# Kernel optimization log

Measured on AMD Instinct MI355X. Metric: run time of the kernel, lower is better.

## Reference

```python
import jax, jax.numpy as jnp
import numpy as np

B, S, D, H = 4, 2048, 1024, 16
DEPTH = D // H
NEG = -1e9


def setup_inputs() -> dict:
    key = jax.random.key(0)
    ks = jax.random.split(key, 9)
    scale = 1.0 / np.sqrt(D)
    x = jax.random.normal(ks[0], (B, S, D), dtype=jnp.float32)
    # causal additive mask: 1 where future positions (masked), 0 elsewhere
    mask = jnp.triu(jnp.ones((S, S), dtype=jnp.float32), k=1)[None, None, :, :]
    wq = jax.random.normal(ks[1], (D, D), dtype=jnp.float32) * scale
    bq = jnp.zeros((D,), dtype=jnp.float32)
    wk = jax.random.normal(ks[2], (D, D), dtype=jnp.float32) * scale
    bk = jnp.zeros((D,), dtype=jnp.float32)
    wv = jax.random.normal(ks[3], (D, D), dtype=jnp.float32) * scale
    bv = jnp.zeros((D,), dtype=jnp.float32)
    wo = jax.random.normal(ks[4], (D, D), dtype=jnp.float32) * scale
    bo = jnp.zeros((D,), dtype=jnp.float32)
    return {"x": x, "mask": mask, "wq": wq, "bq": bq, "wk": wk, "bk": bk,
            "wv": wv, "bv": bv, "wo": wo, "bo": bo}


def _split_heads(t):
    # [B, S, D] -> [B, H, S, depth]
    return t.reshape(B, S, H, DEPTH).transpose(0, 2, 1, 3)


def reference(x, mask, wq, bq, wk, bk, wv, bv, wo, bo):
    q = _split_heads(x @ wq.T + bq)
    k = _split_heads(x @ wk.T + bk)
    v = _split_heads(x @ wv.T + bv)
    scores = jnp.einsum('bhqd,bhkd->bhqk', q, k) / jnp.sqrt(jnp.float32(DEPTH))
    scores = scores + mask * NEG
    attn = jax.nn.softmax(scores, axis=-1)
    out = jnp.einsum('bhqk,bhkd->bhqd', attn, v)  # [B, H, S, depth]
    out = out.transpose(0, 2, 1, 3).reshape(B, S, D)
    return out @ wo.T + bo
```

## Files before the change

### kernel.cpp

```cpp
#include <hip/hip_runtime.h>
#include <hip/hip_bf16.h>
#include <stdint.h>

typedef __attribute__((ext_vector_type(8))) short short8;
typedef __attribute__((ext_vector_type(4))) float f32x4;
typedef __attribute__((ext_vector_type(16))) float f32x16;

#define AS1 __attribute__((address_space(1)))
#define AS3 __attribute__((address_space(3)))

constexpr int Bc = 4, Sc = 2048, Dc = 1024, Hc = 16;

__device__ __forceinline__ unsigned short f2b(float x) {
  __hip_bfloat16 h = __float2bfloat16(x);
  return *reinterpret_cast<unsigned short*>(&h);
}

__device__ __forceinline__ uint32_t cvtpk(float lo, float hi) {
  uint32_t r;
  asm("v_cvt_pk_bf16_f32 %0, %1, %2" : "=v"(r) : "v"(lo), "v"(hi));
  return r;
}

__device__ __forceinline__ void glds16(const void* g, void* l) {
  __builtin_amdgcn_global_load_lds((const AS1 uint32_t*)g, (AS3 uint32_t*)l, 16, 0, 0);
}

__global__ void cast_f32_bf16_x4(const float* __restrict__ in,
                                 unsigned short* __restrict__ out, int n4) {
  int i = blockIdx.x * blockDim.x + threadIdx.x;
  if (i >= n4) return;
  float4 a = ((const float4*)in)[i];
  ushort4 o;
  o.x = f2b(a.x); o.y = f2b(a.y); o.z = f2b(a.z); o.w = f2b(a.w);
  ((ushort4*)out)[i] = o;
}

template<int MODE>
__device__ __forceinline__ void gemm128(
    const unsigned short* __restrict__ A, const unsigned short* __restrict__ W,
    const float* __restrict__ bias, void* __restrict__ outp,
    int m0, int n0, unsigned short* lA, unsigned short* lB)
{
  const int tid = threadIdx.x;
  const int w = tid >> 6, lane = tid & 63;
  const int g = lane >> 4, c = lane & 15;
  const int wr = w >> 1, wc = w & 1;

  f32x4 acc[4][4];
#pragma unroll
  for (int i = 0; i < 4; ++i)
#pragma unroll
    for (int j = 0; j < 4; ++j) acc[i][j] = f32x4{0.f, 0.f, 0.f, 0.f};

  const int srow = lane >> 2;
  const int schunk = (lane & 3) * 8;

  for (int k0 = 0; k0 < 1024; k0 += 32) {
#pragma unroll
    for (int i = 0; i < 2; ++i) {
      int row = i * 64 + w * 16 + srow;
      glds16(A + (size_t)(m0 + row) * 1024 + k0 + schunk,
             (char*)lA + i * 4096 + w * 1024);
      glds16(W + (size_t)(n0 + row) * 1024 + k0 + schunk,
             (char*)lB + i * 4096 + w * 1024);
    }
    __syncthreads();

    short8 aF[4], bF[4];
#pragma unroll
    for (int mt = 0; mt < 4; ++mt) {
      int row = wr * 64 + mt * 16 + c;
      aF[mt] = *(const short8*)&lA[row * 32 + g * 8];
    }
#pragma unroll
    for (int nt = 0; nt < 4; ++nt) {
      int row = wc * 64 + nt * 16 + c;
      bF[nt] = *(const short8*)&lB[row * 32 + g * 8];
    }
#pragma unroll
    for (int mt = 0; mt < 4; ++mt)
#pragma unroll
      for (int nt = 0; nt < 4; ++nt)
        acc[mt][nt] = __builtin_amdgcn_mfma_f32_16x16x32_bf16(aF[mt], bF[nt],
                                                              acc[mt][nt], 0, 0, 0);
    __syncthreads();
  }

#pragma unroll
  for (int mt = 0; mt < 4; ++mt) {
    int mg = m0 + wr * 64 + mt * 16 + 4 * g;
#pragma unroll
    for (int nt = 0; nt < 4; ++nt) {
      int ng = n0 + wc * 64 + nt * 16 + c;
      float bb_ = bias[ng];
      if constexpr (MODE == 0) {
        unsigned short* o = (unsigned short*)outp;
#pragma unroll
        for (int r = 0; r < 4; ++r)
          o[(size_t)(mg + r) * 1024 + ng] = f2b(acc[mt][nt][r] + bb_);
      } else if constexpr (MODE == 1) {
        unsigned short* o = (unsigned short*)outp;
        int bb = mg >> 11, s0 = mg & 2047;
        int hh = ng >> 6, dd = ng & 63;
        ushort4 pk;
        pk.x = f2b(acc[mt][nt][0] + bb_);
        pk.y = f2b(acc[mt][nt][1] + bb_);
        pk.z = f2b(acc[mt][nt][2] + bb_);
        pk.w = f2b(acc[mt][nt][3] + bb_);
        *(ushort4*)&o[(((size_t)bb * Hc + hh) * 64 + dd) * Sc + s0] = pk;
      } else {
        float* o = (float*)outp;
#pragma unroll
        for (int r = 0; r < 4; ++r)
          o[(size_t)(mg + r) * 1024 + ng] = acc[mt][nt][r] + bb_;
      }
    }
  }
}

__global__ __launch_bounds__(256) void qkv_gemm(
    const unsigned short* __restrict__ xb,
    const unsigned short* __restrict__ wqb, const unsigned short* __restrict__ wkb,
    const unsigned short* __restrict__ wvb,
    const float* __restrict__ bq, const float* __restrict__ bk,
    const float* __restrict__ bv,
    unsigned short* __restrict__ qo, unsigned short* __restrict__ ko,
    unsigned short* __restrict__ vto)
{
  __shared__ unsigned short lA[128 * 32], lB[128 * 32];
  int which = blockIdx.x >> 3;
  int n0 = (blockIdx.x & 7) * 128;
  int m0 = blockIdx.y * 128;
  if (which == 0)      gemm128<0>(xb, wqb, bq, qo, m0, n0, lA, lB);
  else if (which == 1) gemm128<0>(xb, wkb, bk, ko, m0, n0, lA, lB);
  else                 gemm128<1>(xb, wvb, bv, vto, m0, n0, lA, lB);
}

__global__ __launch_bounds__(256) void out_gemm(
    const unsigned short* __restrict__ ao, const unsigned short* __restrict__ wob,
    const float* __restrict__ bo, float* __restrict__ out)
{
  __shared__ unsigned short lA[128 * 32], lB[128 * 32];
  gemm128<2>(ao, wob, bo, out, blockIdx.y * 128, blockIdx.x * 128, lA, lB);
}

__global__ __launch_bounds__(256, 2) void attn_kernel(
    const unsigned short* __restrict__ qg, const unsigned short* __restrict__ kg,
    const unsigned short* __restrict__ vtg, unsigned short* __restrict__ ao)
{
  __shared__ unsigned short lK[2][64 * 64];
  __shared__ unsigned short lV[2][64 * 64];

  const int bh = blockIdx.x;
  const int qlo = blockIdx.y, qhi = 15 - qlo;
  const int b = bh >> 4, h = bh & 15;
  const int tid = threadIdx.x, w = tid >> 6, lane = tid & 63;
  const int qr = lane & 31, hi = lane >> 5;
  const int qb2[2] = { qlo * 128 + 32 * w, qhi * 128 + 32 * w };
  constexpr float CE = 0.125f * 1.44269504f;

  short8 qB[2][4];
#pragma unroll
  for (int qi = 0; qi < 2; ++qi) {
    const unsigned short* qp = qg + (size_t)(b * Sc + qb2[qi] + qr) * Dc + h * 64 + 8 * hi;
#pragma unroll
    for (int i = 0; i < 4; ++i)
      qB[qi][i] = *(const short8*)(qp + 16 * i);
  }

  float m_[2] = { -3e38f, -3e38f }, lv[2] = { 0.f, 0.f };
  f32x16 oT[2][2];
#pragma unroll
  for (int qi = 0; qi < 2; ++qi)
#pragma unroll
    for (int n = 0; n < 2; ++n)
#pragma unroll
      for (int r = 0; r < 16; ++r) oT[qi][n][r] = 0.f;

  const int srow8 = lane >> 3;
  const int sslot = lane & 7;
  const unsigned short* kb_ = kg + (size_t)b * Sc * Dc + h * 64;
  const unsigned short* vb_ = vtg + (size_t)bh * 64 * Sc;

  auto stage = [&](int buf, int t) {
    const int kv0 = t * 64;
#pragma unroll
    for (int i = 0; i < 2; ++i) {
      int row = i * 32 + w * 8 + srow8;
      int gch = sslot ^ (row & 7);
      glds16(kb_ + (size_t)(kv0 + row) * Dc + gch * 8,
             (char*)lK[buf] + i * 4096 + w * 1024);
      glds16(vb_ + (size_t)row * Sc + kv0 + gch * 8,
             (char*)lV[buf] + i * 4096 + w * 1024);
    }
  };

  const int ntl = 2 * (qhi + 1);
  stage(0, 0);
  asm volatile("s_waitcnt vmcnt(0)" ::: "memory");
  __builtin_amdgcn_s_barrier();
  asm volatile("" ::: "memory");

  for (int t = 0; t < ntl; ++t) {
    const int cur = t & 1;
    const int kv0 = t * 64;
    if (t + 1 < ntl) stage(cur ^ 1, t + 1);

    if (kv0 <= qb2[1] + 31) {
      short8 kA[2][4];
#pragma unroll
      for (int kblk = 0; kblk < 2; ++kblk) {
        const int row = kblk * 32 + qr;
        const int swz = (row & 7) << 4;
#pragma unroll
        for (int i = 0; i < 4; ++i)
          kA[kblk][i] = *(const short8*)((const char*)lK[cur] + row * 128 +
                          (((2 * i + hi) * 16) ^ swz));
      }

      short8 pB[2][4];
      bool act[2];
#pragma unroll
      for (int qi = 0; qi < 2; ++qi) {
        const int qbase = qb2[qi];
        act[qi] = (kv0 <= qbase + 31);
        if (!act[qi]) continue;

        f32x16 sT[2];
        __builtin_amdgcn_s_setprio(1);
#pragma unroll
        for (int kblk = 0; kblk < 2; ++kblk) {
          f32x16 s;
#pragma unroll
          for (int r = 0; r < 16; ++r) s[r] = 0.f;
#pragma unroll
          for (int i = 0; i < 4; ++i)
            s = __builtin_amdgcn_mfma_f32_32x32x16_bf16(kA[kblk][i], qB[qi][i],
                                                        s, 0, 0, 0);
          sT[kblk] = s;
        }
        __builtin_amdgcn_s_setprio(0);

        if (kv0 + 63 > qbase) {
          const int q = qbase + qr;
#pragma unroll
          for (int kblk = 0; kblk < 2; ++kblk)
#pragma unroll
            for (int r = 0; r < 16; ++r) {
              int k = kv0 + kblk * 32 + (r & 3) + 8 * (r >> 2) + 4 * hi;
              if (k > q) sT[kblk][r] = -1e30f;
            }
        }

        float mx = sT[0][0];
#pragma unroll
        for (int r = 1; r < 16; ++r) mx = fmaxf(mx, sT[0][r]);
#pragma unroll
        for (int r = 0; r < 16; ++r) mx = fmaxf(mx, sT[1][r]);
        mx = fmaxf(mx, __shfl_xor(mx, 32));

        if (!__all(mx <= m_[qi] + 64.f)) {
          const float mo = m_[qi];
          const float mn = fmaxf(mo, mx);
          const float sf = __builtin_amdgcn_exp2f((mo - mn) * CE);
          m_[qi] = mn;
          lv[qi] *= sf;
#pragma unroll
          for (int n = 0; n < 2; ++n)
#pragma unroll
            for (int r = 0; r < 16; ++r) oT[qi][n][r] *= sf;
        }
        const float mc = m_[qi] * CE;
        float ls = 0.f;
#pragma unroll
        for (int kblk = 0; kblk < 2; ++kblk)
#pragma unroll
          for (int r = 0; r < 16; ++r) {
            float p = __builtin_amdgcn_exp2f(sT[kblk][r] * CE - mc);
            sT[kblk][r] = p;
            ls += p;
          }
        lv[qi] += ls;

#pragma unroll
        for (int kblk = 0; kblk < 2; ++kblk) {
          uint32_t pk[4][2];
#pragma unroll
          for (int qp = 0; qp < 4; ++qp)
#pragma unroll
            for (int rp = 0; rp < 2; ++rp)
              pk[qp][rp] = cvtpk(sT[kblk][4 * qp + 2 * rp],
                                 sT[kblk][4 * qp + 2 * rp + 1]);
#pragma unroll
          for (int m2 = 0; m2 < 2; ++m2) {
            uint32_t s0 = hi ? pk[2 * m2][0] : pk[2 * m2 + 1][0];
            uint32_t s1 = hi ? pk[2 * m2][1] : pk[2 * m2 + 1][1];
            uint32_t r0 = __shfl_xor(s0, 32);
            uint32_t r1 = __shfl_xor(s1, 32);
            uint32_t w0 = hi ? r0 : pk[2 * m2][0];
            uint32_t w1 = hi ? r1 : pk[2 * m2][1];
            uint32_t w2 = hi ? pk[2 * m2 + 1][0] : r0;
            uint32_t w3 = hi ? pk[2 * m2 + 1][1] : r1;
            uint32_t tmp[4] = { w0, w1, w2, w3 };
            pB[qi][2 * kblk + m2] = *(const short8*)tmp;
          }
        }
      }

      short8 vA[2][4];
#pragma unroll
      for (int n = 0; n < 2; ++n) {
        const int row = 32 * n + qr;
        const int swz = (row & 7) << 4;
#pragma unroll
        for (int m = 0; m < 4; ++m)
          vA[n][m] = *(const short8*)((const char*)lV[cur] + row * 128 +
                       (((2 * m + hi) * 16) ^ swz));
      }

      __builtin_amdgcn_s_setprio(1);
#pragma unroll
      for (int qi = 0; qi < 2; ++qi) {
        if (!act[qi]) continue;
#pragma unroll
        for (int n = 0; n < 2; ++n)
#pragma unroll
          for (int m = 0; m < 4; ++m)
            oT[qi][n] = __builtin_amdgcn_mfma_f32_32x32x16_bf16(
                vA[n][m], pB[qi][m], oT[qi][n], 0, 0, 0);
      }
      __builtin_amdgcn_s_setprio(0);
    }

    asm volatile("s_waitcnt vmcnt(0)" ::: "memory");
    __builtin_amdgcn_s_barrier();
    asm volatile("" ::: "memory");
  }

#pragma unroll
  for (int qi = 0; qi < 2; ++qi) {
    float l = lv[qi] + __shfl_xor(lv[qi], 32);
    float inv = 1.0f / l;
    const int qrow = qb2[qi] + qr;
    unsigned short* op = ao + (size_t)(b * Sc + qrow) * Dc + h * 64;
#pragma unroll
    for (int n = 0; n < 2; ++n)
#pragma unroll
      for (int rg = 0; rg < 4; ++rg) {
        ushort4 pkv;
        pkv.x = f2b(oT[qi][n][4 * rg + 0] * inv);
        pkv.y = f2b(oT[qi][n][4 * rg + 1] * inv);
        pkv.z = f2b(oT[qi][n][4 * rg + 2] * inv);
        pkv.w = f2b(oT[qi][n][4 * rg + 3] * inv);
        *(ushort4*)(op + 32 * n + 8 * rg + 4 * hi) = pkv;
      }
  }
}

extern "C" void kernel_launch(void* const* d_in, const int* in_sizes, int n_in,
                              void* d_out, int out_size, void* d_ws, size_t ws_size,
                              hipStream_t stream) {
  const float* x  = (const float*)d_in[0];
  const float* wq = (const float*)d_in[2];
  const float* bq = (const float*)d_in[3];
  const float* wk = (const float*)d_in[4];
  const float* bk = (const float*)d_in[5];
  const float* wv = (const float*)d_in[6];
  const float* bv = (const float*)d_in[7];
  const float* wo = (const float*)d_in[8];
  const float* bo = (const float*)d_in[9];
  float* out = (float*)d_out;

  char* ws = (char*)d_ws;
  unsigned short* xb  = (unsigned short*)(ws);
  unsigned short* wqb = (unsigned short*)(ws + 16777216);
  unsigned short* wkb = (unsigned short*)(ws + 18874368);
  unsigned short* wvb = (unsigned short*)(ws + 20971520);
  unsigned short* wob = (unsigned short*)(ws + 23068672);
  unsigned short* qb  = (unsigned short*)(ws + 25165824);
  unsigned short* kb  = (unsigned short*)(ws + 41943040);
  unsigned short* vtb = (unsigned short*)(ws + 58720256);
  unsigned short* aob = (unsigned short*)(ws + 75497472);

  cast_f32_bf16_x4<<<8192, 256, 0, stream>>>(x, xb, 2097152);
  cast_f32_bf16_x4<<<1024, 256, 0, stream>>>(wq, wqb, 262144);
  cast_f32_bf16_x4<<<1024, 256, 0, stream>>>(wk, wkb, 262144);
  cast_f32_bf16_x4<<<1024, 256, 0, stream>>>(wv, wvb, 262144);
  cast_f32_bf16_x4<<<1024, 256, 0, stream>>>(wo, wob, 262144);

  qkv_gemm<<<dim3(24, 64), 256, 0, stream>>>(xb, wqb, wkb, wvb, bq, bk, bv,
                                             qb, kb, vtb);
  attn_kernel<<<dim3(64, 8), 256, 0, stream>>>(qb, kb, vtb, aob);
  out_gemm<<<dim3(8, 64), 256, 0, stream>>>(aob, wob, bo, out);
}
```

Baseline: 183.6 us.

## Double-buffer GEMM LDS staging with XOR swizzle and merge weight casts

The shared GEMM routine now uses two LDS buffers, prefetching the next K-slice with global_load_lds while the current one feeds MFMA. Explicit vmcnt waits and raw barriers replace __syncthreads. The 16-byte chunks are XOR-swizzled by row to cut LDS bank conflicts on fragment reads. The four weight cast launches are merged into one kernel. LDS use doubles per block, which may lower occupancy, and the manual waitcnt ordering is fragile.

After: 184.7 us. Within noise of the previous version (+0.6%).

```diff
diff --git a/kernel.cpp b/kernel.cpp
--- a/kernel.cpp
+++ b/kernel.cpp
@@ -36,11 +36,25 @@
   ((ushort4*)out)[i] = o;
 }
 
+__global__ void cast_w4(const float* __restrict__ wq, const float* __restrict__ wk,
+                        const float* __restrict__ wv, const float* __restrict__ wo,
+                        unsigned short* __restrict__ oq, unsigned short* __restrict__ ok,
+                        unsigned short* __restrict__ ov, unsigned short* __restrict__ oo) {
+  int which = blockIdx.y;
+  const float* in = which == 0 ? wq : which == 1 ? wk : which == 2 ? wv : wo;
+  unsigned short* out = which == 0 ? oq : which == 1 ? ok : which == 2 ? ov : oo;
+  int i = blockIdx.x * blockDim.x + threadIdx.x;
+  float4 a = ((const float4*)in)[i];
+  ushort4 o;
+  o.x = f2b(a.x); o.y = f2b(a.y); o.z = f2b(a.z); o.w = f2b(a.w);
+  ((ushort4*)out)[i] = o;
+}
+
 template<int MODE>
 __device__ __forceinline__ void gemm128(
     const unsigned short* __restrict__ A, const unsigned short* __restrict__ W,
     const float* __restrict__ bias, void* __restrict__ outp,
-    int m0, int n0, unsigned short* lA, unsigned short* lB)
+    int m0, int n0, unsigned short (*lA)[128 * 32], unsigned short (*lB)[128 * 32])
 {
   const int tid = threadIdx.x;
   const int w = tid >> 6, lane = tid & 63;
@@ -54,29 +68,43 @@
     for (int j = 0; j < 4; ++j) acc[i][j] = f32x4{0.f, 0.f, 0.f, 0.f};
 
   const int srow = lane >> 2;
-  const int schunk = (lane & 3) * 8;
-
-  for (int k0 = 0; k0 < 1024; k0 += 32) {
+  const int gch = (lane & 3) ^ ((srow >> 1) & 3);
+  const int rslot = (g ^ ((c >> 1) & 3)) * 16;
+
+  auto stage = [&](int buf, int k0) {
 #pragma unroll
     for (int i = 0; i < 2; ++i) {
       int row = i * 64 + w * 16 + srow;
-      glds16(A + (size_t)(m0 + row) * 1024 + k0 + schunk,
-             (char*)lA + i * 4096 + w * 1024);
-      glds16(W + (size_t)(n0 + row) * 1024 + k0 + schunk,
-             (char*)lB + i * 4096 + w * 1024);
-    }
-    __syncthreads();
+      glds16(A + (size_t)(m0 + row) * 1024 + k0 + gch * 8,
+             (char*)lA[buf] + i * 4096 + w * 1024);
+      glds16(W + (size_t)(n0 + row) * 1024 + k0 + gch * 8,
+             (char*)lB[buf] + i * 4096 + w * 1024);
+    }
+  };
+
+  stage(0, 0);
+
+  for (int t = 0; t < 32; ++t) {
+    const int cur = t & 1;
+    if (t + 1 < 32) {
+      stage(cur ^ 1, (t + 1) * 32);
+      asm volatile("s_waitcnt vmcnt(4)" ::: "memory");
+    } else {
+      asm volatile("s_waitcnt vmcnt(0)" ::: "memory");
+    }
+    __builtin_amdgcn_s_barrier();
+    asm volatile("" ::: "memory");
 
     short8 aF[4], bF[4];
 #pragma unroll
     for (int mt = 0; mt < 4; ++mt) {
       int row = wr * 64 + mt * 16 + c;
-      aF[mt] = *(const short8*)&lA[row * 32 + g * 8];
+      aF[mt] = *(const short8*)((const char*)lA[cur] + row * 64 + rslot);
     }
 #pragma unroll
     for (int nt = 0; nt < 4; ++nt) {
       int row = wc * 64 + nt * 16 + c;
-      bF[nt] = *(const short8*)&lB[row * 32 + g * 8];
+      bF[nt] = *(const short8*)((const char*)lB[cur] + row * 64 + rslot);
     }
 #pragma unroll
     for (int mt = 0; mt < 4; ++mt)
@@ -84,7 +112,9 @@
       for (int nt = 0; nt < 4; ++nt)
         acc[mt][nt] = __builtin_amdgcn_mfma_f32_16x16x32_bf16(aF[mt], bF[nt],
                                                               acc[mt][nt], 0, 0, 0);
-    __syncthreads();
+    asm volatile("" ::: "memory");
+    __builtin_amdgcn_s_barrier();
+    asm volatile("" ::: "memory");
   }
 
 #pragma unroll
@@ -128,7 +158,7 @@
     unsigned short* __restrict__ qo, unsigned short* __restrict__ ko,
     unsigned short* __restrict__ vto)
 {
-  __shared__ unsigned short lA[128 * 32], lB[128 * 32];
+  __shared__ unsigned short lA[2][128 * 32], lB[2][128 * 32];
   int which = blockIdx.x >> 3;
   int n0 = (blockIdx.x & 7) * 128;
   int m0 = blockIdx.y * 128;
@@ -141,7 +171,7 @@
     const unsigned short* __restrict__ ao, const unsigned short* __restrict__ wob,
     const float* __restrict__ bo, float* __restrict__ out)
 {
-  __shared__ unsigned short lA[128 * 32], lB[128 * 32];
+  __shared__ unsigned short lA[2][128 * 32], lB[2][128 * 32];
   gemm128<2>(ao, wob, bo, out, blockIdx.y * 128, blockIdx.x * 128, lA, lB);
 }
 
@@ -384,10 +414,7 @@
   unsigned short* aob = (unsigned short*)(ws + 75497472);
 
   cast_f32_bf16_x4<<<8192, 256, 0, stream>>>(x, xb, 2097152);
-  cast_f32_bf16_x4<<<1024, 256, 0, stream>>>(wq, wqb, 262144);
-  cast_f32_bf16_x4<<<1024, 256, 0, stream>>>(wk, wkb, 262144);
-  cast_f32_bf16_x4<<<1024, 256, 0, stream>>>(wv, wvb, 262144);
-  cast_f32_bf16_x4<<<1024, 256, 0, stream>>>(wo, wob, 262144);
+  cast_w4<<<dim3(1024, 4), 256, 0, stream>>>(wq, wk, wv, wo, wqb, wkb, wvb, wob);
 
   qkv_gemm<<<dim3(24, 64), 256, 0, stream>>>(xb, wqb, wkb, wvb, bq, bk, bv,
                                              qb, kb, vtb);
```
